# Performance work log

Hardware: AMD Instinct MI355X
Metric: run time of the kernel (lower is better)

The kernel has to match this reference:

```python
import jax, jax.numpy as jnp
import numpy as np

HID = 512
J = 64
NEG = -1e9


def _gru_cell(x, h, Wih, Whh, bih, bhh):
    # PyTorch GRUCell: gates stacked as (r, z, n) along first dim of (3H, in)
    gi = Wih @ x + bih          # (3H,)
    gh = Whh @ h + bhh          # (3H,)
    r = jax.nn.sigmoid(gi[:HID] + gh[:HID])
    z = jax.nn.sigmoid(gi[HID:2 * HID] + gh[HID:2 * HID])
    n = jnp.tanh(gi[2 * HID:] + r * gh[2 * HID:])
    return (1.0 - z) * n + z * h


def setup_inputs() -> dict:
    key = jax.random.key(0)
    ks = jax.random.split(key, 8)
    T = 4096
    state_dim = 2 * J  # input is state[t][1:]
    d = {
        "state": jax.random.normal(ks[0], (T, state_dim + 1), dtype=jnp.float32),
        "h_prev": jnp.zeros((2, HID), dtype=jnp.float32),
        "mask": jax.random.randint(ks[1], (J, J), 0, 2, dtype=jnp.int32),
        "Wih0": jax.random.normal(ks[2], (3 * HID, state_dim), dtype=jnp.float32) * 0.05,
        "Whh0": jax.random.normal(ks[3], (3 * HID, HID), dtype=jnp.float32) * 0.04,
        "bih0": jnp.zeros((3 * HID,), dtype=jnp.float32),
        "bhh0": jnp.zeros((3 * HID,), dtype=jnp.float32),
        "Wih1": jax.random.normal(ks[4], (3 * HID, HID), dtype=jnp.float32) * 0.04,
        "Whh1": jax.random.normal(ks[5], (3 * HID, HID), dtype=jnp.float32) * 0.04,
        "bih1": jnp.zeros((3 * HID,), dtype=jnp.float32),
        "bhh1": jnp.zeros((3 * HID,), dtype=jnp.float32),
        "Wfc": jax.random.normal(ks[6], (J * J, HID), dtype=jnp.float32) * 0.06,
        "bfc": jnp.zeros((J * J,), dtype=jnp.float32),
    }
    return d


def reference(state, h_prev, mask, Wih0, Whh0, bih0, bhh0,
              Wih1, Whh1, bih1, bhh1, Wfc, bfc):
    xs = state[:, 1:]  # drop leading element, matches state[t][1:]

    def step(hs, x_t):
        h0 = _gru_cell(x_t, hs[0], Wih0, Whh0, bih0, bhh0)
        h1 = _gru_cell(h0, hs[1], Wih1, Whh1, bih1, bhh1)
        new = jnp.stack([h0, h1])
        return new, h1

    h_next, h_list = jax.lax.scan(step, h_prev, xs)  # h_list: (T, HID)
    logits = jax.nn.relu(h_list @ Wfc.T + bfc)       # (T, J*J)
    logits = logits.reshape(-1, J, J)
    logits = jnp.where(mask == 0, jnp.float32(NEG), logits)
    return logits, h_next
```

## Files before the change

### kernel.cpp

```cpp
#include <hip/hip_runtime.h>
#include <stdint.h>

#define TSTEPS   4096
#define NEG_VAL  -1000000000.0f
#define NWG_SCAN 96
#define G0WG     32
#define RINGN    32

#define GI0_OFF   0
#define H1_OFF    (TSTEPS*1536*4)
#define RING0_OFF (H1_OFF + TSTEPS*512*4)
#define RING1_OFF (RING0_OFF + RINGN*512*8)
#define ARR_OFF   (RING1_OFF + RINGN*512*8)
#define WS_NEED   ((size_t)ARR_OFF + RINGN*64)

static __device__ __forceinline__ unsigned long long ld_a64(const unsigned long long* p){
  return __hip_atomic_load(p, __ATOMIC_RELAXED, __HIP_MEMORY_SCOPE_AGENT);
}
static __device__ __forceinline__ void st_a64(unsigned long long* p, unsigned long long v){
  __hip_atomic_store(p, v, __ATOMIC_RELAXED, __HIP_MEMORY_SCOPE_AGENT);
}
static __device__ __forceinline__ float sigmoidf_(float x){
  return 1.0f / (1.0f + __expf(-x));
}
static __device__ __forceinline__ float tanhf_(float x){
  float ax = fabsf(x);
  float e  = __expf(-2.0f*ax);
  float t  = (1.0f - e) / (1.0f + e);
  return copysignf(t, x);
}

static __device__ __forceinline__ void spin_to_lds(const unsigned long long* ring, int slot,
                                                   unsigned want, int lane, float* dst,
                                                   long* budget){
  const unsigned long long* bp = ring + (size_t)slot*512 + lane;
  unsigned long long v[8];
  for(;;){
    #pragma unroll
    for (int j=0;j<8;++j) v[j] = ld_a64(bp + j*64);
    bool ok = true;
    #pragma unroll
    for (int j=0;j<8;++j) ok = ok && ((unsigned)(v[j]>>32) == want);
    if (ok) break;
    if (--(*budget) < 0) break;
  }
  #pragma unroll
  for (int j=0;j<8;++j) dst[j*64+lane] = __uint_as_float((unsigned)v[j]);
}

__global__ __launch_bounds__(384,1) void gru_scan(
    const float* __restrict__ gi0,
    const float* __restrict__ hprev,
    const float* __restrict__ Whh0,
    const float* __restrict__ Wih1,
    const float* __restrict__ Whh1,
    const float* __restrict__ bhh0,
    const float* __restrict__ bih1,
    const float* __restrict__ bhh1,
    float* __restrict__ H1hist,
    unsigned long long* ring0,
    unsigned long long* ring1,
    unsigned* arr,
    float* __restrict__ hnext)
{
  const int wg   = blockIdx.x;
  const int tid  = threadIdx.x;
  const int wave = tid >> 6;
  const int lane = tid & 63;

  __shared__ float hbuf0[512];
  __shared__ float hbuf1[512];
  __shared__ float sc[64];

  long budget = (1L<<22);

  if (wg < G0WG) {
    const int ibase = wg*16;
    float w[8][8];
    #pragma unroll
    for (int k=0;k<8;++k){
      const int rid = wave*8+k;
      const int g = rid>>4, il = rid&15;
      const float* wp = Whh0 + ((size_t)(g*512 + ibase + il))*512;
      #pragma unroll
      for (int j=0;j<8;++j) w[k][j] = wp[j*64 + lane];
    }
    float hreg=0.f, br=0.f, bz=0.f, bn_=0.f;
    const int mi = ibase + tid;
    if (tid < 16){
      hreg = hprev[mi];
      br  = bhh0[mi]; bz = bhh0[512+mi]; bn_ = bhh0[1024+mi];
    }
    for (int t=0; t<TSTEPS; ++t){
      float gr=0.f, gz=0.f, gn=0.f;
      if (tid < 16){
        const float* gp = gi0 + (size_t)t*1536 + mi;
        gr = gp[0]; gz = gp[512]; gn = gp[1024];
      }
      if (wave == 0){
        if (t == 0){
          #pragma unroll
          for (int j=0;j<8;++j) hbuf0[j*64+lane] = hprev[j*64+lane];
        } else {
          spin_to_lds(ring0, (t-1)&(RINGN-1), (unsigned)t, lane, hbuf0, &budget);
        }
      }
      if (tid==0 && t>=16){
        unsigned* ap = arr + (size_t)((t-16)&(RINGN-1))*16;
        const unsigned expect = (unsigned)NWG_SCAN * (unsigned)(((t-16)>>5)+1);
        while (__hip_atomic_load(ap, __ATOMIC_RELAXED, __HIP_MEMORY_SCOPE_AGENT) < expect){
          if (--budget < 0) break;
        }
      }
      __syncthreads();
      float hj[8];
      #pragma unroll
      for (int j=0;j<8;++j) hj[j] = hbuf0[j*64+lane];
      float acc[8];
      #pragma unroll
      for (int k=0;k<8;++k){
        float a = 0.f;
        #pragma unroll
        for (int j=0;j<8;++j) a = fmaf(w[k][j], hj[j], a);
        #pragma unroll
        for (int off=32; off; off>>=1) a += __shfl_xor(a, off, 64);
        acc[k] = a;
      }
      if (lane == 0){
        #pragma unroll
        for (int k=0;k<8;++k) sc[wave*8+k] = acc[k];
      }
      __syncthreads();
      if (tid < 16){
        const float ghr = sc[tid]    + br;
        const float ghz = sc[16+tid] + bz;
        const float ghn = sc[32+tid] + bn_;
        const float r = sigmoidf_(gr + ghr);
        const float z = sigmoidf_(gz + ghz);
        const float n = tanhf_(gn + r*ghn);
        const float h = (1.f - z)*n + z*hreg;
        hreg = h;
        st_a64(ring0 + (size_t)(t&(RINGN-1))*512 + mi,
               ((unsigned long long)(unsigned)(t+1)<<32) |
               (unsigned long long)__float_as_uint(h));
        if (t == TSTEPS-1) hnext[mi] = h;
      }
      __syncthreads();
      if (tid == 0){
        __hip_atomic_fetch_add(arr + (size_t)(t&(RINGN-1))*16, 1u,
                               __ATOMIC_RELEASE, __HIP_MEMORY_SCOPE_AGENT);
      }
    }
  } else {
    const int wgl = wg - G0WG;
    const int ibase = wgl*8;
    const bool isA = (wave < 3);
    float w[8][8];
    #pragma unroll
    for (int k=0;k<8;++k){
      const int rid = (isA ? wave : (wave-3))*8 + k;
      const int g = rid>>3, il = rid&7;
      const float* W = isA ? Wih1 : Whh1;
      const float* wp = W + ((size_t)(g*512 + ibase + il))*512;
      #pragma unroll
      for (int j=0;j<8;++j) w[k][j] = wp[j*64 + lane];
    }
    float hreg=0.f, bir=0.f,biz=0.f,bin_=0.f, bhr=0.f,bhz=0.f,bhn=0.f;
    const int mi = ibase + tid;
    if (tid < 8){
      hreg = hprev[512+mi];
      bir = bih1[mi]; biz = bih1[512+mi]; bin_ = bih1[1024+mi];
      bhr = bhh1[mi]; bhz = bhh1[512+mi]; bhn  = bhh1[1024+mi];
    }
    for (int s=0; s<TSTEPS; ++s){
      if (wave == 0){
        spin_to_lds(ring0, s&(RINGN-1), (unsigned)(s+1), lane, hbuf0, &budget);
      } else if (wave == 3){
        if (s == 0){
          #pragma unroll
          for (int j=0;j<8;++j) hbuf1[j*64+lane] = hprev[512 + j*64+lane];
        } else {
          spin_to_lds(ring1, (s-1)&(RINGN-1), (unsigned)s, lane, hbuf1, &budget);
        }
      }
      if (tid==0 && s>=16){
        unsigned* ap = arr + (size_t)((s-16)&(RINGN-1))*16;
        const unsigned expect = (unsigned)NWG_SCAN * (unsigned)(((s-16)>>5)+1);
        while (__hip_atomic_load(ap, __ATOMIC_RELAXED, __HIP_MEMORY_SCOPE_AGENT) < expect){
          if (--budget < 0) break;
        }
      }
      __syncthreads();
      const float* hsrc = isA ? hbuf0 : hbuf1;
      float hj[8];
      #pragma unroll
      for (int j=0;j<8;++j) hj[j] = hsrc[j*64+lane];
      float acc[8];
      #pragma unroll
      for (int k=0;k<8;++k){
        float a = 0.f;
        #pragma unroll
        for (int j=0;j<8;++j) a = fmaf(w[k][j], hj[j], a);
        #pragma unroll
        for (int off=32; off; off>>=1) a += __shfl_xor(a, off, 64);
        acc[k] = a;
      }
      if (lane == 0){
        const int base = isA ? (wave*8) : (24 + (wave-3)*8);
        #pragma unroll
        for (int k=0;k<8;++k) sc[base+k] = acc[k];
      }
      __syncthreads();
      if (tid < 8){
        const float gir = sc[tid]    + bir;
        const float giz = sc[8+tid]  + biz;
        const float gin = sc[16+tid] + bin_;
        const float ghr = sc[24+tid] + bhr;
        const float ghz = sc[32+tid] + bhz;
        const float ghn = sc[40+tid] + bhn;
        const float r = sigmoidf_(gir + ghr);
        const float z = sigmoidf_(giz + ghz);
        const float n = tanhf_(gin + r*ghn);
        const float h = (1.f - z)*n + z*hreg;
        hreg = h;
        st_a64(ring1 + (size_t)(s&(RINGN-1))*512 + mi,
               ((unsigned long long)(unsigned)(s+1)<<32) |
               (unsigned long long)__float_as_uint(h));
        H1hist[(size_t)s*512 + mi] = h;
        if (s == TSTEPS-1) hnext[512+mi] = h;
      }
      __syncthreads();
      if (tid == 0){
        __hip_atomic_fetch_add(arr + (size_t)(s&(RINGN-1))*16, 1u,
                               __ATOMIC_RELEASE, __HIP_MEMORY_SCOPE_AGENT);
      }
    }
  }
}

template<int EPI>
__global__ __launch_bounds__(256) void gemm_nt(
    const float* __restrict__ A, int lda,
    const float* __restrict__ B, int ldb,
    float* __restrict__ C, int ldc,
    const float* __restrict__ bias,
    const int* __restrict__ mask,
    int K)
{
  __shared__ __align__(16) float As[32][68];
  __shared__ __align__(16) float Bs[32][68];
  const int bm = blockIdx.y*64, bn = blockIdx.x*64;
  const int tid = threadIdx.x;
  const int tm = tid>>4, tn = tid&15;
  float acc[4][4] = {};
  const int m0 = tid>>2, kk0 = (tid&3)*8;
  for (int k0=0; k0<K; k0+=32){
    #pragma unroll
    for (int j=0;j<8;++j) As[kk0+j][m0] = A[(size_t)(bm+m0)*lda + k0+kk0+j];
    #pragma unroll
    for (int j=0;j<8;++j) Bs[kk0+j][m0] = B[(size_t)(bn+m0)*ldb + k0+kk0+j];
    __syncthreads();
    #pragma unroll
    for (int kk=0;kk<32;++kk){
      const float4 av = *(const float4*)&As[kk][tm*4];
      const float4 bv = *(const float4*)&Bs[kk][tn*4];
      acc[0][0]=fmaf(av.x,bv.x,acc[0][0]); acc[0][1]=fmaf(av.x,bv.y,acc[0][1]);
      acc[0][2]=fmaf(av.x,bv.z,acc[0][2]); acc[0][3]=fmaf(av.x,bv.w,acc[0][3]);
      acc[1][0]=fmaf(av.y,bv.x,acc[1][0]); acc[1][1]=fmaf(av.y,bv.y,acc[1][1]);
      acc[1][2]=fmaf(av.y,bv.z,acc[1][2]); acc[1][3]=fmaf(av.y,bv.w,acc[1][3]);
      acc[2][0]=fmaf(av.z,bv.x,acc[2][0]); acc[2][1]=fmaf(av.z,bv.y,acc[2][1]);
      acc[2][2]=fmaf(av.z,bv.z,acc[2][2]); acc[2][3]=fmaf(av.z,bv.w,acc[2][3]);
      acc[3][0]=fmaf(av.w,bv.x,acc[3][0]); acc[3][1]=fmaf(av.w,bv.y,acc[3][1]);
      acc[3][2]=fmaf(av.w,bv.z,acc[3][2]); acc[3][3]=fmaf(av.w,bv.w,acc[3][3]);
    }
    __syncthreads();
  }
  #pragma unroll
  for (int i=0;i<4;++i){
    #pragma unroll
    for (int j=0;j<4;++j){
      const int mm = bm + tm*4 + i, cc = bn + tn*4 + j;
      float v = acc[i][j] + bias[cc];
      if (EPI){
        v = fmaxf(v, 0.f);
        if (mask[cc] == 0) v = NEG_VAL;
      }
      C[(size_t)mm*ldc + cc] = v;
    }
  }
}

extern "C" void kernel_launch(void* const* d_in, const int* in_sizes, int n_in,
                              void* d_out, int out_size, void* d_ws, size_t ws_size,
                              hipStream_t stream)
{
  const float* state = (const float*)d_in[0];
  const float* hprev = (const float*)d_in[1];
  const int*   mask  = (const int*)d_in[2];
  const float* Wih0  = (const float*)d_in[3];
  const float* Whh0  = (const float*)d_in[4];
  const float* bih0  = (const float*)d_in[5];
  const float* bhh0  = (const float*)d_in[6];
  const float* Wih1  = (const float*)d_in[7];
  const float* Whh1  = (const float*)d_in[8];
  const float* bih1  = (const float*)d_in[9];
  const float* bhh1  = (const float*)d_in[10];
  const float* Wfc   = (const float*)d_in[11];
  const float* bfc   = (const float*)d_in[12];

  if (ws_size < WS_NEED) return;

  float* out = (float*)d_out;
  char*  ws  = (char*)d_ws;
  float* gi0 = (float*)(ws + GI0_OFF);
  float* H1  = (float*)(ws + H1_OFF);
  unsigned long long* ring0 = (unsigned long long*)(ws + RING0_OFF);
  unsigned long long* ring1 = (unsigned long long*)(ws + RING1_OFF);
  unsigned* arr = (unsigned*)(ws + ARR_OFF);

  (void)hipMemsetAsync(ws + RING0_OFF, 0, (size_t)(WS_NEED - RING0_OFF), stream);

  {
    dim3 grid(1536/64, 4096/64);
    gemm_nt<0><<<grid, 256, 0, stream>>>(state+1, 129, Wih0, 128, gi0, 1536,
                                         bih0, nullptr, 128);
  }

  gru_scan<<<NWG_SCAN, 384, 0, stream>>>(gi0, hprev, Whh0, Wih1, Whh1,
                                         bhh0, bih1, bhh1,
                                         H1, ring0, ring1, arr,
                                         out + (size_t)4096*4096);

  {
    dim3 grid(4096/64, 4096/64);
    gemm_nt<1><<<grid, 256, 0, stream>>>(H1, 512, Wfc, 512, out, 4096,
                                         bfc, mask, 512);
  }
}
```

Before: 12.84 ms.

## Fuse GRU scan and FC GEMM into one persistent kernel with fp16 dot products

Replaces the three launches (input GEMM, scan, FC GEMM) with one persistent kernel. It uses 8 workgroups for layer 0, which computes the input projection inline, 16 workgroups for layer 1, and the remaining workgroups pull FC GEMM tiles through a ticket counter as H1 rows become ready. Weights are held in registers as fp16 pairs and combined with fdot2, and hidden states travel through the rings as packed fp16. Gate values are exchanged with DPP and shuffles instead of LDS reductions. The aim is to cut per-step latency and overlap the FC GEMM with the scan, at the cost of fp16 precision loss and more complex spin synchronisation.

```diff
diff --git a/kernel.cpp b/kernel.cpp
--- a/kernel.cpp
+++ b/kernel.cpp
@@ -1,24 +1,40 @@
 #include <hip/hip_runtime.h>
 #include <stdint.h>
 
-#define TSTEPS   4096
-#define NEG_VAL  -1000000000.0f
-#define NWG_SCAN 96
-#define G0WG     32
-#define RINGN    32
-
-#define GI0_OFF   0
-#define H1_OFF    (TSTEPS*1536*4)
-#define RING0_OFF (H1_OFF + TSTEPS*512*4)
-#define RING1_OFF (RING0_OFF + RINGN*512*8)
-#define ARR_OFF   (RING1_OFF + RINGN*512*8)
-#define WS_NEED   ((size_t)ARR_OFF + RINGN*64)
+#define TSTEPS  4096
+#define NEG_VAL -1000000000.0f
+#define L0N 8
+#define L1N 16
+#define SCANWG 24
+#define GRIDWG 256
+
+typedef _Float16 h2 __attribute__((ext_vector_type(2)));
+
+#define H1_OFF     0
+#define RING0_OFF  (TSTEPS*512*4)
+#define RING1_OFF  (RING0_OFF + 32*256*8)
+#define PROGS_OFF  (RING1_OFF + 32*256*8)
+#define PROGH_OFF  (PROGS_OFF + SCANWG*64)
+#define TICK_OFF   (PROGH_OFF + L1N*64)
+#define WS_NEED    ((size_t)TICK_OFF + 64)
 
 static __device__ __forceinline__ unsigned long long ld_a64(const unsigned long long* p){
   return __hip_atomic_load(p, __ATOMIC_RELAXED, __HIP_MEMORY_SCOPE_AGENT);
 }
 static __device__ __forceinline__ void st_a64(unsigned long long* p, unsigned long long v){
   __hip_atomic_store(p, v, __ATOMIC_RELAXED, __HIP_MEMORY_SCOPE_AGENT);
+}
+static __device__ __forceinline__ unsigned ld_u32(const unsigned* p){
+  return __hip_atomic_load(p, __ATOMIC_RELAXED, __HIP_MEMORY_SCOPE_AGENT);
+}
+static __device__ __forceinline__ void st_u32(unsigned* p, unsigned v){
+  __hip_atomic_store(p, v, __ATOMIC_RELAXED, __HIP_MEMORY_SCOPE_AGENT);
+}
+static __device__ __forceinline__ unsigned ld_acq(const unsigned* p){
+  return __hip_atomic_load(p, __ATOMIC_ACQUIRE, __HIP_MEMORY_SCOPE_AGENT);
+}
+static __device__ __forceinline__ void st_rel(unsigned* p, unsigned v){
+  __hip_atomic_store(p, v, __ATOMIC_RELEASE, __HIP_MEMORY_SCOPE_AGENT);
 }
 static __device__ __forceinline__ float sigmoidf_(float x){
   return 1.0f / (1.0f + __expf(-x));
@@ -29,263 +45,290 @@
   float t  = (1.0f - e) / (1.0f + e);
   return copysignf(t, x);
 }
-
-static __device__ __forceinline__ void spin_to_lds(const unsigned long long* ring, int slot,
-                                                   unsigned want, int lane, float* dst,
-                                                   long* budget){
-  const unsigned long long* bp = ring + (size_t)slot*512 + lane;
-  unsigned long long v[8];
-  for(;;){
-    #pragma unroll
-    for (int j=0;j<8;++j) v[j] = ld_a64(bp + j*64);
-    bool ok = true;
-    #pragma unroll
-    for (int j=0;j<8;++j) ok = ok && ((unsigned)(v[j]>>32) == want);
-    if (ok) break;
-    if (--(*budget) < 0) break;
-  }
-  #pragma unroll
-  for (int j=0;j<8;++j) dst[j*64+lane] = __uint_as_float((unsigned)v[j]);
-}
-
-__global__ __launch_bounds__(384,1) void gru_scan(
-    const float* __restrict__ gi0,
+static __device__ __forceinline__ uint32_t pack2h(float a, float b){
+  _Float16 ha = (_Float16)a, hb = (_Float16)b;
+  unsigned short ua = __builtin_bit_cast(unsigned short, ha);
+  unsigned short ub = __builtin_bit_cast(unsigned short, hb);
+  return (uint32_t)ua | ((uint32_t)ub << 16);
+}
+static __device__ __forceinline__ h2 u2h2(uint32_t u){ return __builtin_bit_cast(h2, u); }
+
+template<int CTRL>
+static __device__ __forceinline__ float dppx(float x){
+  return __int_as_float(__builtin_amdgcn_update_dpp(0, __float_as_int(x), CTRL, 0xF, 0xF, true));
+}
+#define DPP_B0 0x00
+#define DPP_B1 0x55
+#define DPP_B2 0xAA
+
+#if __has_builtin(__builtin_amdgcn_fdot2)
+#define FDOT2(a,b,c) __builtin_amdgcn_fdot2((a),(b),(c),false)
+#else
+static __device__ __forceinline__ float FDOT2(h2 a, h2 b, float c){
+  return c + (float)a[0]*(float)b[0] + (float)a[1]*(float)b[1];
+}
+#endif
+
+__global__ __launch_bounds__(256,1) void actor_fused(
+    const float* __restrict__ state,
     const float* __restrict__ hprev,
+    const int*   __restrict__ mask,
+    const float* __restrict__ Wih0,
     const float* __restrict__ Whh0,
+    const float* __restrict__ bih0,
+    const float* __restrict__ bhh0,
     const float* __restrict__ Wih1,
     const float* __restrict__ Whh1,
-    const float* __restrict__ bhh0,
     const float* __restrict__ bih1,
     const float* __restrict__ bhh1,
-    float* __restrict__ H1hist,
+    const float* __restrict__ Wfc,
+    const float* __restrict__ bfc,
+    float* __restrict__ H1,
     unsigned long long* ring0,
     unsigned long long* ring1,
-    unsigned* arr,
+    unsigned* progS,
+    unsigned* progH,
+    unsigned* ticket,
+    float* __restrict__ out,
     float* __restrict__ hnext)
 {
   const int wg   = blockIdx.x;
   const int tid  = threadIdx.x;
-  const int wave = tid >> 6;
+  const int wv   = tid >> 6;
   const int lane = tid & 63;
-
-  __shared__ float hbuf0[512];
-  __shared__ float hbuf1[512];
-  __shared__ float sc[64];
-
-  long budget = (1L<<22);
-
-  if (wg < G0WG) {
-    const int ibase = wg*16;
-    float w[8][8];
-    #pragma unroll
-    for (int k=0;k<8;++k){
-      const int rid = wave*8+k;
-      const int g = rid>>4, il = rid&15;
-      const float* wp = Whh0 + ((size_t)(g*512 + ibase + il))*512;
-      #pragma unroll
-      for (int j=0;j<8;++j) w[k][j] = wp[j*64 + lane];
-    }
-    float hreg=0.f, br=0.f, bz=0.f, bn_=0.f;
-    const int mi = ibase + tid;
-    if (tid < 16){
-      hreg = hprev[mi];
-      br  = bhh0[mi]; bz = bhh0[512+mi]; bn_ = bhh0[1024+mi];
-    }
+  const int c    = lane & 3;
+  const int rg   = lane >> 2;
+
+  __shared__ __align__(16) char smem[17472];
+  uint32_t* hb0 = (uint32_t*)smem;
+  uint32_t* hb1 = hb0 + 512;
+  uint32_t* xb  = hb0 + 1024;
+  long bd = 1L << 22;
+
+  if (wg < L0N){
+    const int obase = wg*64;
+    const int o = obase + wv*16 + rg;
+    const int g = (c < 3) ? c : 2;
+    h2 Wh[256]; h2 Wx[64];
+    {
+      const float4* r4 = (const float4*)(Whh0 + (size_t)(g*512 + o)*512);
+      #pragma unroll
+      for (int i=0;i<128;++i){
+        float4 v = r4[i];
+        Wh[2*i]   = h2{(_Float16)v.x,(_Float16)v.y};
+        Wh[2*i+1] = h2{(_Float16)v.z,(_Float16)v.w};
+      }
+      const float4* x4 = (const float4*)(Wih0 + (size_t)(g*512 + o)*128);
+      #pragma unroll
+      for (int i=0;i<32;++i){
+        float4 v = x4[i];
+        Wx[2*i]   = h2{(_Float16)v.x,(_Float16)v.y};
+        Wx[2*i+1] = h2{(_Float16)v.z,(_Float16)v.w};
+      }
+    }
+    float hreg = hprev[o];
+    const float bh = bhh0[g*512+o], bi = bih0[g*512+o];
+    hb0[tid] = pack2h(hprev[2*tid], hprev[2*tid+1]);
+    if (tid < 64) xb[tid] = pack2h(state[1+2*tid], state[2+2*tid]);
+
     for (int t=0; t<TSTEPS; ++t){
-      float gr=0.f, gz=0.f, gn=0.f;
-      if (tid < 16){
-        const float* gp = gi0 + (size_t)t*1536 + mi;
-        gr = gp[0]; gz = gp[512]; gn = gp[1024];
-      }
-      if (wave == 0){
-        if (t == 0){
-          #pragma unroll
-          for (int j=0;j<8;++j) hbuf0[j*64+lane] = hprev[j*64+lane];
-        } else {
-          spin_to_lds(ring0, (t-1)&(RINGN-1), (unsigned)t, lane, hbuf0, &budget);
-        }
-      }
-      if (tid==0 && t>=16){
-        unsigned* ap = arr + (size_t)((t-16)&(RINGN-1))*16;
-        const unsigned expect = (unsigned)NWG_SCAN * (unsigned)(((t-16)>>5)+1);
-        while (__hip_atomic_load(ap, __ATOMIC_RELAXED, __HIP_MEMORY_SCOPE_AGENT) < expect){
-          if (--budget < 0) break;
-        }
+      if (t > 0){
+        const unsigned long long* p = ring0 + (size_t)((t-1)&31)*256 + tid;
+        unsigned long long v;
+        for(;;){ v = ld_a64(p); if ((unsigned)(v>>32) == (unsigned)t) break;
+                 if (--bd < 0) break; }
+        hb0[(t&1)*256 + tid] = (uint32_t)v;
+        if (tid < 64){
+          const float* xr = state + (size_t)t*129 + 1;
+          xb[(t&1)*64 + tid] = pack2h(xr[2*tid], xr[2*tid+1]);
+        }
+        if (tid == 0 && (t&7)==0 && t >= 32){
+          for (int w2=0; w2<SCANWG; ++w2){
+            const unsigned* pp = progS + w2*16;
+            while ((int)ld_u32(pp) < t-20){ if (--bd < 0) break; }
+          }
+        }
+        if (tid == 2 && (t&7)==0) st_u32(progS + wg*16, (unsigned)t);
       }
       __syncthreads();
-      float hj[8];
-      #pragma unroll
-      for (int j=0;j<8;++j) hj[j] = hbuf0[j*64+lane];
-      float acc[8];
-      #pragma unroll
-      for (int k=0;k<8;++k){
-        float a = 0.f;
+
+      const uint32_t* hs = hb0 + (t&1)*256;
+      float acch = 0.f;
+      #pragma unroll
+      for (int i=0;i<64;++i){
+        uint4 hv = *(const uint4*)(hs + 4*i);
+        acch = FDOT2(Wh[4*i+0], u2h2(hv.x), acch);
+        acch = FDOT2(Wh[4*i+1], u2h2(hv.y), acch);
+        acch = FDOT2(Wh[4*i+2], u2h2(hv.z), acch);
+        acch = FDOT2(Wh[4*i+3], u2h2(hv.w), acch);
+      }
+      const uint32_t* xs = xb + (t&1)*64;
+      float accx = 0.f;
+      #pragma unroll
+      for (int i=0;i<16;++i){
+        uint4 xv = *(const uint4*)(xs + 4*i);
+        accx = FDOT2(Wx[4*i+0], u2h2(xv.x), accx);
+        accx = FDOT2(Wx[4*i+1], u2h2(xv.y), accx);
+        accx = FDOT2(Wx[4*i+2], u2h2(xv.z), accx);
+        accx = FDOT2(Wx[4*i+3], u2h2(xv.w), accx);
+      }
+      const float A = acch + bh;
+      const float B = accx + bi;
+      const float Ar = dppx<DPP_B0>(A), Az = dppx<DPP_B1>(A), An = dppx<DPP_B2>(A);
+      const float Br = dppx<DPP_B0>(B), Bz = dppx<DPP_B1>(B), Bn = dppx<DPP_B2>(B);
+      const float r = sigmoidf_(Br + Ar);
+      const float z = sigmoidf_(Bz + Az);
+      const float n = tanhf_(Bn + r*An);
+      const float h = (1.f - z)*n + z*hreg;
+      hreg = h;
+      const float h1v = __shfl_xor(h, 4, 64);
+      if ((lane & 7) == 0){
+        st_a64(ring0 + (size_t)(t&31)*256 + (obase>>1) + wv*8 + (rg>>1),
+               ((unsigned long long)(unsigned)(t+1) << 32) | pack2h(h, h1v));
+      }
+      if (t == TSTEPS-1 && c == 0) hnext[o] = h;
+    }
+  } else if (wg < SCANWG){
+    const int q = wg - L0N;
+    const int qbase = q*32;
+    const int o = qbase + wv*8 + (rg>>1);
+    const int slot = rg & 1;
+    const int g = (c < 3) ? c : 2;
+    h2 W[256];
+    {
+      const float* M = slot ? Wih1 : Whh1;
+      const float4* r4 = (const float4*)(M + (size_t)(g*512 + o)*512);
+      #pragma unroll
+      for (int i=0;i<128;++i){
+        float4 v = r4[i];
+        W[2*i]   = h2{(_Float16)v.x,(_Float16)v.y};
+        W[2*i+1] = h2{(_Float16)v.z,(_Float16)v.w};
+      }
+    }
+    float hreg = hprev[512+o];
+    const float bb = slot ? bih1[g*512+o] : bhh1[g*512+o];
+    hb1[tid] = pack2h(hprev[512+2*tid], hprev[512+2*tid+1]);
+
+    for (int s=0; s<TSTEPS; ++s){
+      {
+        const unsigned long long* p = ring0 + (size_t)(s&31)*256 + tid;
+        unsigned long long v;
+        for(;;){ v = ld_a64(p); if ((unsigned)(v>>32) == (unsigned)(s+1)) break;
+                 if (--bd < 0) break; }
+        hb0[(s&1)*256 + tid] = (uint32_t)v;
+      }
+      if (s > 0){
+        const unsigned long long* p = ring1 + (size_t)((s-1)&31)*256 + tid;
+        unsigned long long v;
+        for(;;){ v = ld_a64(p); if ((unsigned)(v>>32) == (unsigned)s) break;
+                 if (--bd < 0) break; }
+        hb1[(s&1)*256 + tid] = (uint32_t)v;
+      }
+      if (tid == 0 && (s&7)==0 && s >= 32){
+        for (int w2=L0N; w2<SCANWG; ++w2){
+          const unsigned* pp = progS + w2*16;
+          while ((int)ld_u32(pp) < s-20){ if (--bd < 0) break; }
+        }
+      }
+      if (tid == 2 && (s&7)==0 && s > 0) st_u32(progS + wg*16, (unsigned)s);
+      if (tid == 3 && (s&15)==0 && s > 0) st_rel(progH + q*16, (unsigned)(s-1));
+      __syncthreads();
+
+      const uint32_t* hs = (slot ? hb0 : hb1) + (s&1)*256;
+      float acc = 0.f;
+      #pragma unroll
+      for (int i=0;i<64;++i){
+        uint4 hv = *(const uint4*)(hs + 4*i);
+        acc = FDOT2(W[4*i+0], u2h2(hv.x), acc);
+        acc = FDOT2(W[4*i+1], u2h2(hv.y), acc);
+        acc = FDOT2(W[4*i+2], u2h2(hv.z), acc);
+        acc = FDOT2(W[4*i+3], u2h2(hv.w), acc);
+      }
+      const float A = acc + bb;
+      const float Ar = dppx<DPP_B0>(A), Az = dppx<DPP_B1>(A), An = dppx<DPP_B2>(A);
+      const float Xr = __shfl_xor(Ar, 4, 64);
+      const float Xz = __shfl_xor(Az, 4, 64);
+      const float Xn = __shfl_xor(An, 4, 64);
+      const float hh_r = slot ? Xr : Ar, ih_r = slot ? Ar : Xr;
+      const float hh_z = slot ? Xz : Az, ih_z = slot ? Az : Xz;
+      const float hh_n = slot ? Xn : An, ih_n = slot ? An : Xn;
+      const float r = sigmoidf_(ih_r + hh_r);
+      const float z = sigmoidf_(ih_z + hh_z);
+      const float n = tanhf_(ih_n + r*hh_n);
+      const float h = (1.f - z)*n + z*hreg;
+      hreg = h;
+      const float ho1 = __shfl_xor(h, 8, 64);
+      if ((lane & 15) == 0){
+        st_a64(ring1 + (size_t)(s&31)*256 + (qbase>>1) + wv*4 + (rg>>2),
+               ((unsigned long long)(unsigned)(s+1) << 32) | pack2h(h, ho1));
+      }
+      if ((lane & 7) == 0) H1[(size_t)s*512 + o] = h;
+      if (s == TSTEPS-1 && (lane & 7) == 0) hnext[512+o] = h;
+    }
+    __syncthreads();
+    if (tid == 3) st_rel(progH + q*16, (unsigned)TSTEPS);
+  } else {
+    float* Asd = (float*)smem;
+    float* Bsd = Asd + 32*68;
+    int*   comm = (int*)(smem + 17408);
+    const int tm = tid>>4, tn = tid&15, m0 = tid>>2, kk0 = (tid&3)*8;
+    for(;;){
+      if (tid == 0) comm[0] = (int)atomicAdd(ticket, 1u);
+      __syncthreads();
+      const int tau = comm[0];
+      if (tau >= 4096) break;
+      const int bm = tau >> 6, bn = tau & 63;
+      if (tid == 0){
+        const unsigned need = (unsigned)(bm*64 + 64);
+        for(;;){
+          unsigned mn = 0xFFFFFFFFu;
+          for (int w2=0; w2<L1N; ++w2){
+            unsigned v = ld_acq(progH + w2*16);
+            mn = (v < mn) ? v : mn;
+          }
+          if (mn >= need) break;
+          __builtin_amdgcn_s_sleep(32);
+          if (--bd < 0) break;
+        }
+      }
+      __syncthreads();
+
+      const float* A = H1 + (size_t)bm*64*512;
+      const float* B = Wfc + (size_t)bn*64*512;
+      float acc[4][4] = {};
+      for (int k0=0; k0<512; k0+=32){
         #pragma unroll
-        for (int j=0;j<8;++j) a = fmaf(w[k][j], hj[j], a);
+        for (int j=0;j<8;++j) Asd[(kk0+j)*68 + m0] = A[(size_t)m0*512 + k0+kk0+j];
         #pragma unroll
-        for (int off=32; off; off>>=1) a += __shfl_xor(a, off, 64);
-        acc[k] = a;
-      }
-      if (lane == 0){
+        for (int j=0;j<8;++j) Bsd[(kk0+j)*68 + m0] = B[(size_t)m0*512 + k0+kk0+j];
+        __syncthreads();
         #pragma unroll
-        for (int k=0;k<8;++k) sc[wave*8+k] = acc[k];
-      }
-      __syncthreads();
-      if (tid < 16){
-        const float ghr = sc[tid]    + br;
-        const float ghz = sc[16+tid] + bz;
-        const float ghn = sc[32+tid] + bn_;
-        const float r = sigmoidf_(gr + ghr);
-        const float z = sigmoidf_(gz + ghz);
-        const float n = tanhf_(gn + r*ghn);
-        const float h = (1.f - z)*n + z*hreg;
-        hreg = h;
-        st_a64(ring0 + (size_t)(t&(RINGN-1))*512 + mi,
-               ((unsigned long long)(unsigned)(t+1)<<32) |
-               (unsigned long long)__float_as_uint(h));
-        if (t == TSTEPS-1) hnext[mi] = h;
-      }
-      __syncthreads();
-      if (tid == 0){
-        __hip_atomic_fetch_add(arr + (size_t)(t&(RINGN-1))*16, 1u,
-                               __ATOMIC_RELEASE, __HIP_MEMORY_SCOPE_AGENT);
-      }
-    }
-  } else {
-    const int wgl = wg - G0WG;
-    const int ibase = wgl*8;
-    const bool isA = (wave < 3);
-    float w[8][8];
-    #pragma unroll
-    for (int k=0;k<8;++k){
-      const int rid = (isA ? wave : (wave-3))*8 + k;
-      const int g = rid>>3, il = rid&7;
-      const float* W = isA ? Wih1 : Whh1;
-      const float* wp = W + ((size_t)(g*512 + ibase + il))*512;
-      #pragma unroll
-      for (int j=0;j<8;++j) w[k][j] = wp[j*64 + lane];
-    }
-    float hreg=0.f, bir=0.f,biz=0.f,bin_=0.f, bhr=0.f,bhz=0.f,bhn=0.f;
-    const int mi = ibase + tid;
-    if (tid < 8){
-      hreg = hprev[512+mi];
-      bir = bih1[mi]; biz = bih1[512+mi]; bin_ = bih1[1024+mi];
-      bhr = bhh1[mi]; bhz = bhh1[512+mi]; bhn  = bhh1[1024+mi];
-    }
-    for (int s=0; s<TSTEPS; ++s){
-      if (wave == 0){
-        spin_to_lds(ring0, s&(RINGN-1), (unsigned)(s+1), lane, hbuf0, &budget);
-      } else if (wave == 3){
-        if (s == 0){
-          #pragma unroll
-          for (int j=0;j<8;++j) hbuf1[j*64+lane] = hprev[512 + j*64+lane];
-        } else {
-          spin_to_lds(ring1, (s-1)&(RINGN-1), (unsigned)s, lane, hbuf1, &budget);
-        }
-      }
-      if (tid==0 && s>=16){
-        unsigned* ap = arr + (size_t)((s-16)&(RINGN-1))*16;
-        const unsigned expect = (unsigned)NWG_SCAN * (unsigned)(((s-16)>>5)+1);
-        while (__hip_atomic_load(ap, __ATOMIC_RELAXED, __HIP_MEMORY_SCOPE_AGENT) < expect){
-          if (--budget < 0) break;
-        }
-      }
-      __syncthreads();
-      const float* hsrc = isA ? hbuf0 : hbuf1;
-      float hj[8];
-      #pragma unroll
-      for (int j=0;j<8;++j) hj[j] = hsrc[j*64+lane];
-      float acc[8];
-      #pragma unroll
-      for (int k=0;k<8;++k){
-        float a = 0.f;
+        for (int kk=0;kk<32;++kk){
+          const float4 av = *(const float4*)&Asd[kk*68 + tm*4];
+          const float4 bv = *(const float4*)&Bsd[kk*68 + tn*4];
+          acc[0][0]=fmaf(av.x,bv.x,acc[0][0]); acc[0][1]=fmaf(av.x,bv.y,acc[0][1]);
+          acc[0][2]=fmaf(av.x,bv.z,acc[0][2]); acc[0][3]=fmaf(av.x,bv.w,acc[0][3]);
+          acc[1][0]=fmaf(av.y,bv.x,acc[1][0]); acc[1][1]=fmaf(av.y,bv.y,acc[1][1]);
+          acc[1][2]=fmaf(av.y,bv.z,acc[1][2]); acc[1][3]=fmaf(av.y,bv.w,acc[1][3]);
+          acc[2][0]=fmaf(av.z,bv.x,acc[2][0]); acc[2][1]=fmaf(av.z,bv.y,acc[2][1]);
+          acc[2][2]=fmaf(av.z,bv.z,acc[2][2]); acc[2][3]=fmaf(av.z,bv.w,acc[2][3]);
+          acc[3][0]=fmaf(av.w,bv.x,acc[3][0]); acc[3][1]=fmaf(av.w,bv.y,acc[3][1]);
+          acc[3][2]=fmaf(av.w,bv.z,acc[3][2]); acc[3][3]=fmaf(av.w,bv.w,acc[3][3]);
+        }
+        __syncthreads();
+      }
+      #pragma unroll
+      for (int i=0;i<4;++i){
         #pragma unroll
-        for (int j=0;j<8;++j) a = fmaf(w[k][j], hj[j], a);
-        #pragma unroll
-        for (int off=32; off; off>>=1) a += __shfl_xor(a, off, 64);
-        acc[k] = a;
-      }
-      if (lane == 0){
-        const int base = isA ? (wave*8) : (24 + (wave-3)*8);
-        #pragma unroll
-        for (int k=0;k<8;++k) sc[base+k] = acc[k];
-      }
-      __syncthreads();
-      if (tid < 8){
-        const float gir = sc[tid]    + bir;
-        const float giz = sc[8+tid]  + biz;
-        const float gin = sc[16+tid] + bin_;
-        const float ghr = sc[24+tid] + bhr;
-        const float ghz = sc[32+tid] + bhz;
-        const float ghn = sc[40+tid] + bhn;
-        const float r = sigmoidf_(gir + ghr);
-        const float z = sigmoidf_(giz + ghz);
-        const float n = tanhf_(gin + r*ghn);
-        const float h = (1.f - z)*n + z*hreg;
-        hreg = h;
-        st_a64(ring1 + (size_t)(s&(RINGN-1))*512 + mi,
-               ((unsigned long long)(unsigned)(s+1)<<32) |
-               (unsigned long long)__float_as_uint(h));
-        H1hist[(size_t)s*512 + mi] = h;
-        if (s == TSTEPS-1) hnext[512+mi] = h;
-      }
-      __syncthreads();
-      if (tid == 0){
-        __hip_atomic_fetch_add(arr + (size_t)(s&(RINGN-1))*16, 1u,
-                               __ATOMIC_RELEASE, __HIP_MEMORY_SCOPE_AGENT);
-      }
-    }
-  }
-}
-
-template<int EPI>
-__global__ __launch_bounds__(256) void gemm_nt(
-    const float* __restrict__ A, int lda,
-    const float* __restrict__ B, int ldb,
-    float* __restrict__ C, int ldc,
-    const float* __restrict__ bias,
-    const int* __restrict__ mask,
-    int K)
-{
-  __shared__ __align__(16) float As[32][68];
-  __shared__ __align__(16) float Bs[32][68];
-  const int bm = blockIdx.y*64, bn = blockIdx.x*64;
-  const int tid = threadIdx.x;
-  const int tm = tid>>4, tn = tid&15;
-  float acc[4][4] = {};
-  const int m0 = tid>>2, kk0 = (tid&3)*8;
-  for (int k0=0; k0<K; k0+=32){
-    #pragma unroll
-    for (int j=0;j<8;++j) As[kk0+j][m0] = A[(size_t)(bm+m0)*lda + k0+kk0+j];
-    #pragma unroll
-    for (int j=0;j<8;++j) Bs[kk0+j][m0] = B[(size_t)(bn+m0)*ldb + k0+kk0+j];
-    __syncthreads();
-    #pragma unroll
-    for (int kk=0;kk<32;++kk){
-      const float4 av = *(const float4*)&As[kk][tm*4];
-      const float4 bv = *(const float4*)&Bs[kk][tn*4];
-      acc[0][0]=fmaf(av.x,bv.x,acc[0][0]); acc[0][1]=fmaf(av.x,bv.y,acc[0][1]);
-      acc[0][2]=fmaf(av.x,bv.z,acc[0][2]); acc[0][3]=fmaf(av.x,bv.w,acc[0][3]);
-      acc[1][0]=fmaf(av.y,bv.x,acc[1][0]); acc[1][1]=fmaf(av.y,bv.y,acc[1][1]);
-      acc[1][2]=fmaf(av.y,bv.z,acc[1][2]); acc[1][3]=fmaf(av.y,bv.w,acc[1][3]);
-      acc[2][0]=fmaf(av.z,bv.x,acc[2][0]); acc[2][1]=fmaf(av.z,bv.y,acc[2][1]);
-      acc[2][2]=fmaf(av.z,bv.z,acc[2][2]); acc[2][3]=fmaf(av.z,bv.w,acc[2][3]);
-      acc[3][0]=fmaf(av.w,bv.x,acc[3][0]); acc[3][1]=fmaf(av.w,bv.y,acc[3][1]);
-      acc[3][2]=fmaf(av.w,bv.z,acc[3][2]); acc[3][3]=fmaf(av.w,bv.w,acc[3][3]);
-    }
-    __syncthreads();
-  }
-  #pragma unroll
-  for (int i=0;i<4;++i){
-    #pragma unroll
-    for (int j=0;j<4;++j){
-      const int mm = bm + tm*4 + i, cc = bn + tn*4 + j;
-      float v = acc[i][j] + bias[cc];
-      if (EPI){
-        v = fmaxf(v, 0.f);
-        if (mask[cc] == 0) v = NEG_VAL;
-      }
-      C[(size_t)mm*ldc + cc] = v;
+        for (int j=0;j<4;++j){
+          const int mm = bm*64 + tm*4 + i;
+          const int cc = bn*64 + tn*4 + j;
+          float v = acc[i][j] + bfc[cc];
+          v = fmaxf(v, 0.f);
+          if (mask[cc] == 0) v = NEG_VAL;
+          out[(size_t)mm*4096 + cc] = v;
+        }
+      }
     }
   }
 }
@@ -312,28 +355,18 @@
 
   float* out = (float*)d_out;
   char*  ws  = (char*)d_ws;
-  float* gi0 = (float*)(ws + GI0_OFF);
   float* H1  = (float*)(ws + H1_OFF);
   unsigned long long* ring0 = (unsigned long long*)(ws + RING0_OFF);
   unsigned long long* ring1 = (unsigned long long*)(ws + RING1_OFF);
-  unsigned* arr = (unsigned*)(ws + ARR_OFF);
+  unsigned* progS  = (unsigned*)(ws + PROGS_OFF);
+  unsigned* progH  = (unsigned*)(ws + PROGH_OFF);
+  unsigned* ticket = (unsigned*)(ws + TICK_OFF);
 
   (void)hipMemsetAsync(ws + RING0_OFF, 0, (size_t)(WS_NEED - RING0_OFF), stream);
 
-  {
-    dim3 grid(1536/64, 4096/64);
-    gemm_nt<0><<<grid, 256, 0, stream>>>(state+1, 129, Wih0, 128, gi0, 1536,
-                                         bih0, nullptr, 128);
-  }
-
-  gru_scan<<<NWG_SCAN, 384, 0, stream>>>(gi0, hprev, Whh0, Wih1, Whh1,
-                                         bhh0, bih1, bhh1,
-                                         H1, ring0, ring1, arr,
-                                         out + (size_t)4096*4096);
-
-  {
-    dim3 grid(4096/64, 4096/64);
-    gemm_nt<1><<<grid, 256, 0, stream>>>(H1, 512, Wfc, 512, out, 4096,
-                                         bfc, mask, 512);
-  }
-}
+  actor_fused<<<GRIDWG, 256, 0, stream>>>(
+      state, hprev, mask, Wih0, Whh0, bih0, bhh0,
+      Wih1, Whh1, bih1, bhh1, Wfc, bfc,
+      H1, ring0, ring1, progS, progH, ticket,
+      out, out + (size_t)4096*4096);
+}
```

New measurement: 44.64 ms. +247.7%, slower.
